# Kernel optimization log

Measured on AMD Instinct MI355X. Metric: run time of the kernel, lower is better.

The kernel has to match this reference:

```python
import jax, jax.numpy as jnp
import numpy as np

B, P, ENC, DEC, EMB, ATT, FFN, V, MAXLEN = 64, 196, 512, 512, 256, 128, 1024, 2000, 160
T = MAXLEN - 1
EPS = 1e-5

def _k(i):
    return jax.random.fold_in(jax.random.key(0), i)

def _w(i, shape):
    return jax.random.normal(_k(i), shape, jnp.float32) * 0.02

def setup_inputs() -> dict:
    lens = jnp.concatenate([jnp.array([MAXLEN]), jax.random.randint(_k(2), (B - 1,), 2, MAXLEN + 1)])
    return {
        "encoder_out": jax.random.normal(_k(0), (B, P, ENC), jnp.float32),
        "encoded_captions": jax.random.randint(_k(1), (B, MAXLEN), 0, V),
        "caption_lengths": lens,
        "enc_att_w": _w(3, (ATT, ENC)), "enc_att_b": _w(4, (ATT,)),
        "dec_att_w": _w(5, (ATT, DEC)), "dec_att_b": _w(6, (ATT,)),
        "full_att_w": _w(7, (1, ATT)), "full_att_b": _w(8, (1,)),
        "gate_w1": _w(9, (ATT, DEC)), "gate_b1": _w(10, (ATT,)),
        "gate_w2": _w(11, (1, ATT)), "gate_b2": _w(12, (1,)),
        "emb": jax.random.uniform(_k(13), (V, EMB), jnp.float32, -0.1, 0.1),
        "gru1_wih": _w(14, (3 * DEC, EMB + ENC)), "gru1_whh": _w(15, (3 * DEC, DEC)),
        "gru1_bih": _w(16, (3 * DEC,)), "gru1_bhh": _w(17, (3 * DEC,)),
        "gru2_wih": _w(18, (3 * DEC, DEC)), "gru2_whh": _w(19, (3 * DEC, DEC)),
        "gru2_bih": _w(20, (3 * DEC,)), "gru2_bhh": _w(21, (3 * DEC,)),
        "proj_w": _w(22, (DEC, EMB + ENC)), "proj_b": _w(23, (DEC,)),
        "ln1_g": jnp.ones((DEC,), jnp.float32), "ln1_b": jnp.zeros((DEC,), jnp.float32),
        "ln2_g": jnp.ones((DEC,), jnp.float32), "ln2_b": jnp.zeros((DEC,), jnp.float32),
        "ffn_w1": _w(24, (FFN, DEC)), "ffn_b1": jnp.zeros((FFN,), jnp.float32),
        "ffn_w2": _w(25, (V, FFN)), "ffn_b2": jnp.zeros((V,), jnp.float32),
    }

def _gru(x, h, wih, whh, bih, bhh):
    gi = x @ wih.T + bih
    gh = h @ whh.T + bhh
    ir, iz, ig = jnp.split(gi, 3, axis=-1)
    hr, hz, hg = jnp.split(gh, 3, axis=-1)
    r = jax.nn.sigmoid(ir + hr)
    z = jax.nn.sigmoid(iz + hz)
    n = jnp.tanh(ig + r * hg)
    return (1.0 - z) * n + z * h

def _ln(x, g, b):
    m = x.mean(-1, keepdims=True)
    v = x.var(-1, keepdims=True)
    return (x - m) / jnp.sqrt(v + EPS) * g + b

def _decode(encoder_out, encoded_captions, caption_lengths,
            enc_att_w, enc_att_b, dec_att_w, dec_att_b, full_att_w, full_att_b,
            gate_w1, gate_b1, gate_w2, gate_b2, emb,
            gru1_wih, gru1_whh, gru1_bih, gru1_bhh,
            gru2_wih, gru2_whh, gru2_bih, gru2_bhh,
            proj_w, proj_b, ln1_g, ln1_b, ln2_g, ln2_b,
            ffn_w1, ffn_b1, ffn_w2, ffn_b2):
    # sort by caption length descending (packed-sequence style)
    order = jnp.argsort(-caption_lengths)
    enc = encoder_out[order]                       # [B,P,ENC]
    caps = encoded_captions[order]                 # [B,MAXLEN]
    dec_lens = caption_lengths[order] - 1          # [B]
    att1 = enc @ enc_att_w.T + enc_att_b           # [B,P,ATT] (loop-invariant)
    xs = jnp.swapaxes(emb[caps[:, :T]], 0, 1)      # [T,B,EMB] teacher forcing (p=1.0)
    masks = (jnp.arange(T)[:, None] < dec_lens[None, :]).astype(enc.dtype)  # [T,B]

    def step(carry, inp):
        h1, h2 = carry
        x_t, m = inp                               # [B,EMB], [B]
        att2 = h2 @ dec_att_w.T + dec_att_b        # [B,ATT]
        e = (jax.nn.relu(att1 + att2[:, None, :]) @ full_att_w.T + full_att_b)[..., 0]  # [B,P]
        alpha = jax.nn.softmax(e, axis=1)
        awe = jnp.einsum('bpe,bp->be', enc, alpha)
        gate = jax.nn.sigmoid(jax.nn.relu(h2 @ gate_w1.T + gate_b1) @ gate_w2.T + gate_b2)  # [B,1]
        awe = awe * gate
        gin = jnp.concatenate([x_t, awe], axis=1)  # [B,EMB+ENC]
        h1_new = _gru(gin, h1, gru1_wih, gru1_whh, gru1_bih, gru1_bhh)
        h1_res = _ln(h1_new + gin @ proj_w.T + proj_b, ln1_g, ln1_b)
        h2_new = _gru(h1_res, h2, gru2_wih, gru2_whh, gru2_bih, gru2_bhh)
        h2_res = _ln(h2_new + h1_res, ln2_g, ln2_b)  # dropout is identity (eval)
        preds = jax.nn.relu(h2_res @ ffn_w1.T + ffn_b1) @ ffn_w2.T + ffn_b2  # [B,V]
        mc = m[:, None]
        h1 = jnp.where(mc > 0, h1_new, h1)
        h2 = jnp.where(mc > 0, h2_new, h2)
        return (h1, h2), (preds * mc, alpha * mc)

    h0 = jnp.zeros((enc.shape[0], DEC), enc.dtype)
    _, (preds, alphas) = jax.lax.scan(step, (h0, h0), (xs, masks))
    predictions = jnp.swapaxes(preds, 0, 1)        # [B,T,V]
    alphas = jnp.swapaxes(alphas, 0, 1)            # [B,T,P]
    return predictions, caps, dec_lens, alphas, order

def reference(encoder_out, encoded_captions, caption_lengths,
              enc_att_w, enc_att_b, dec_att_w, dec_att_b, full_att_w, full_att_b,
              gate_w1, gate_b1, gate_w2, gate_b2, emb,
              gru1_wih, gru1_whh, gru1_bih, gru1_bhh,
              gru2_wih, gru2_whh, gru2_bih, gru2_bhh,
              proj_w, proj_b, ln1_g, ln1_b, ln2_g, ln2_b,
              ffn_w1, ffn_b1, ffn_w2, ffn_b2):
    return _decode(encoder_out, encoded_captions, caption_lengths,
                   enc_att_w, enc_att_b, dec_att_w, dec_att_b, full_att_w, full_att_b,
                   gate_w1, gate_b1, gate_w2, gate_b2, emb,
                   gru1_wih, gru1_whh, gru1_bih, gru1_bhh,
                   gru2_wih, gru2_whh, gru2_bih, gru2_bhh,
                   proj_w, proj_b, ln1_g, ln1_b, ln2_g, ln2_b,
                   ffn_w1, ffn_b1, ffn_w2, ffn_b2)
```

## Files before the change

### kernel.cpp

```cpp
#include <hip/hip_runtime.h>
#include <math.h>

#define B 64
#define P 196
#define ENCD 512
#define DECD 512
#define EMBD 256
#define ATTD 128
#define FFND 1024
#define VV 2000
#define MAXLEN 160
#define TSTEPS 159
#define EPS 1e-5f

#define OUT_PRED ((size_t)0)
#define OUT_CAPS ((size_t)(B * TSTEPS * VV))
#define OUT_DECL (OUT_CAPS + (size_t)(B * MAXLEN))
#define OUT_ALPH (OUT_DECL + (size_t)B)
#define OUT_ORDR (OUT_ALPH + (size_t)(B * TSTEPS * P))


struct Ctx {
  const float* enc; const int* caps_in; const int* lens_in;
  const float* eaw; const float* eab; const float* daw; const float* dab;
  const float* faw; const float* fab;
  const float* gw1; const float* gb1; const float* gw2; const float* gb2;
  const float* emb;
  const float* wih1; const float* whh1; const float* bih1; const float* bhh1;
  const float* wih2; const float* whh2; const float* bih2; const float* bhh2;
  const float* projw; const float* projb;
  const float* ln1g; const float* ln1b; const float* ln2g; const float* ln2b;
  const float* fw1; const float* fb1; const float* fw2; const float* fb2;
  int* leafs; int* root;
  int* order_i; int* declen; int* caps_s;
  float* EaT; float* att1;
  float* h1; float* h2; float* v1; float* v2;
  float* gin; float* fgr; float* gh1g; float* gh2g; float* att2acc;
  float* stats1; float* stats2;
  float* WA; float* WB; float* WC; float* WD; float* Watt;
  float* Sf; float* cbf; float* Sg; float* cbg;
  float* out;
};

__device__ __forceinline__ float sigf(float x) { return 1.f / (1.f + __expf(-x)); }

__device__ __forceinline__ float ld4(const float* p) {
  unsigned int u = __hip_atomic_load((const unsigned int*)p, __ATOMIC_RELAXED, __HIP_MEMORY_SCOPE_AGENT);
  return __uint_as_float(u);
}
__device__ __forceinline__ void st4(float* p, float v) {
  __hip_atomic_store((unsigned int*)p, __float_as_uint(v), __ATOMIC_RELAXED, __HIP_MEMORY_SCOPE_AGENT);
}
__device__ __forceinline__ void st8(float* p, float a, float b2) {
  unsigned long long v = ((unsigned long long)__float_as_uint(b2) << 32) | (unsigned long long)__float_as_uint(a);
  __hip_atomic_store((unsigned long long*)p, v, __ATOMIC_RELAXED, __HIP_MEMORY_SCOPE_AGENT);
}
__device__ __forceinline__ void atomF(float* p, float v) {
  __hip_atomic_fetch_add(p, v, __ATOMIC_RELAXED, __HIP_MEMORY_SCOPE_AGENT);
}
__device__ __forceinline__ float4 ldg16(const float* p) {
  float4 d;
  asm volatile("global_load_dwordx4 %0, %1, off sc0 sc1" : "=v"(d) : "v"(p));
  return d;
}
__device__ __forceinline__ void vmwait() { asm volatile("s_waitcnt vmcnt(0)" ::: "memory"); }

__device__ __forceinline__ float pfl(const float* p) {
  float v;
  asm volatile("global_load_dword %0, %1, off" : "=v"(v) : "v"(p));
  return v;
}
__device__ __forceinline__ void pfsink8(float a, float b, float c2, float d,
                                        float e, float f, float g2, float h) {
  asm volatile("" :: "v"(a), "v"(b), "v"(c2), "v"(d), "v"(e), "v"(f), "v"(g2), "v"(h));
}
__device__ __forceinline__ void pfsink2(float a, float b) {
  asm volatile("" :: "v"(a), "v"(b));
}

__device__ __forceinline__ unsigned short tobf(float x) {
  unsigned int u = __float_as_uint(x);
  u += 0x7fffu + ((u >> 16) & 1u);
  return (unsigned short)(u >> 16);
}
__device__ __forceinline__ float frombf(unsigned short s) {
  return __uint_as_float(((unsigned int)s) << 16);
}


__global__ void k_order(Ctx c) {
  __shared__ int lens[B];
  int tid = threadIdx.x;
  lens[tid] = c.lens_in[tid];
  __syncthreads();
  int li = lens[tid];
  int pos = 0;
  for (int j = 0; j < B; ++j) {
    int lj = lens[j];
    pos += (lj > li || (lj == li && j < tid)) ? 1 : 0;
  }
  c.order_i[pos] = tid;
  c.declen[pos] = li - 1;
  c.out[OUT_ORDR + pos] = (float)tid;
  c.out[OUT_DECL + pos] = (float)(li - 1);
}

__global__ __launch_bounds__(256) void k_caps(Ctx c) {
  int idx = blockIdx.x * 256 + threadIdx.x;
  if (idx < B * MAXLEN) {
    int b = idx / MAXLEN, t = idx - b * MAXLEN;
    int v = c.caps_in[c.order_i[b] * MAXLEN + t];
    c.caps_s[idx] = v;
    c.out[OUT_CAPS + idx] = (float)v;
  }
}

__global__ __launch_bounds__(256) void k_eat(Ctx c) {
  int idx = blockIdx.x * 256 + threadIdx.x;
  if (idx < 128 * 512) {
    int k = idx >> 7, d = idx & 127;
    c.EaT[(size_t)k * 128 + d] = c.eaw[(size_t)d * 512 + k];
  }
}

__global__ __launch_bounds__(256) void k_att1(Ctx c) {
  __shared__ float Xs[8 * 512];
  int tid = threadIdx.x;
  int r0 = blockIdx.x * 8;
  for (int idx = tid; idx < 8 * 512; idx += 256) {
    int rr = idx >> 9, k = idx & 511;
    int r = r0 + rr;
    int b = r / P, p = r - b * P;
    int ob = c.order_i[b];
    Xs[idx] = c.enc[((size_t)(ob * P + p)) * ENCD + k];
  }
  __syncthreads();
  int d = tid >> 1, kh = tid & 1;
  float acc[8];
#pragma unroll
  for (int rr = 0; rr < 8; ++rr) acc[rr] = 0.f;
  int kbase = kh * 256;
  for (int k = 0; k < 256; ++k) {
    float w = c.EaT[(size_t)(kbase + k) * 128 + d];
#pragma unroll
    for (int rr = 0; rr < 8; ++rr) acc[rr] = fmaf(w, Xs[rr * 512 + kbase + k], acc[rr]);
  }
#pragma unroll
  for (int rr = 0; rr < 8; ++rr) {
    acc[rr] += __shfl_xor(acc[rr], 1);
    if (kh == 0) c.att1[(size_t)(r0 + rr) * 128 + d] = acc[rr];
  }
}

__global__ __launch_bounds__(256) void k_wpa(Ctx c) {
  int s = blockIdx.x;
  float* dst = c.WA + (size_t)s * 65536;
  for (int idx = threadIdx.x; idx < 65536; idx += 256) {
    int kb = idx >> 9, r = idx & 511, cc = r >> 2, jj = r & 3;
    int col = s * 128 + cc, k = kb * 4 + jj;
    float v;
    if (col < 1536) v = c.whh1[(size_t)col * 512 + k];
    else if (col < 3072) v = c.whh2[(size_t)(col - 1536) * 512 + k];
    else v = c.ln2g[k] * c.fw1[(size_t)(col - 3072) * 512 + k];
    dst[idx] = v;
  }
}

__global__ __launch_bounds__(256) void k_wpb(Ctx c) {
  int s = blockIdx.x;
  float* dst = c.WB + (size_t)s * 49152;
  for (int idx = threadIdx.x; idx < 49152; idx += 256) {
    int kb = idx >> 8, r = idx & 255, cc = r >> 2, jj = r & 3;
    int u = s * 64 + cc, k = kb * 4 + jj;
    int d = u >> 2, comp = u & 3;
    dst[idx] = (comp < 3) ? c.wih1[(size_t)(comp * 512 + d) * 768 + k]
                          : c.projw[(size_t)d * 768 + k];
  }
}

__global__ __launch_bounds__(256) void k_wpc(Ctx c) {
  int s = blockIdx.x;
  float* dst = c.WC + (size_t)s * 24576;
  for (int idx = threadIdx.x; idx < 24576; idx += 256) {
    int kb = idx / 192, r = idx - kb * 192, cc = r >> 2, jj = r & 3;
    int u = s * 48 + cc, k = kb * 4 + jj;
    int d = u / 3, comp = u - d * 3;
    dst[idx] = c.ln1g[k] * c.wih2[(size_t)(comp * 512 + d) * 512 + k];
  }
}

__global__ __launch_bounds__(256) void k_wpd(Ctx c) {
  int s = blockIdx.x;
  float* dst = c.WD + (size_t)s * 65536;
  for (int idx = threadIdx.x; idx < 65536; idx += 256) {
    int kb = idx >> 8, r = idx & 255, cc = r >> 2, jj = r & 3;
    int vcol = s * 64 + cc, k = kb * 4 + jj;
    dst[idx] = (vcol < 2000) ? c.fw2[(size_t)vcol * 1024 + k] : 0.f;
  }
}

__global__ __launch_bounds__(256) void k_watt(Ctx c) {
  int ks = blockIdx.x;
  float* dst = c.Watt + (size_t)ks * 16384;
  for (int idx = threadIdx.x; idx < 16384; idx += 256) {
    int kb = idx >> 10, r = idx & 1023, cc = r >> 2, jj = r & 3;
    int k = ks * 64 + kb * 4 + jj;
    dst[idx] = (cc < 128) ? c.daw[(size_t)cc * 512 + k] : c.gw1[(size_t)(cc - 128) * 512 + k];
  }
}

__global__ __launch_bounds__(256) void k_consts(Ctx c) {
  __shared__ float r1[256], r2[256];
  int i = blockIdx.x, tid = threadIdx.x;
  float a = 0.f, b2 = 0.f;
  if (i < 1024) {
    const float* w = c.fw1 + (size_t)i * 512;
    for (int k = tid; k < 512; k += 256) { a = fmaf(c.ln2g[k], w[k], a); b2 = fmaf(c.ln2b[k], w[k], b2); }
  } else {
    const float* w = c.wih2 + (size_t)(i - 1024) * 512;
    for (int k = tid; k < 512; k += 256) { a = fmaf(c.ln1g[k], w[k], a); b2 = fmaf(c.ln1b[k], w[k], b2); }
  }
  r1[tid] = a; r2[tid] = b2;
  __syncthreads();
  for (int s = 128; s > 0; s >>= 1) {
    if (tid < s) { r1[tid] += r1[tid + s]; r2[tid] += r2[tid + s]; }
    __syncthreads();
  }
  if (tid == 0) {
    if (i < 1024) { c.Sf[i] = r1[0]; c.cbf[i] = r2[0] + c.fb1[i]; }
    else { c.Sg[i - 1024] = r1[0]; c.cbg[i - 1024] = r2[0] + c.bih2[i - 1024]; }
  }
}


__device__ __forceinline__ void gridbar(int* leafs, int* root, int ph) {
  __builtin_amdgcn_s_waitcnt(0);
  __syncthreads();
  if (threadIdx.x == 0) {
    int old = __hip_atomic_fetch_add(&leafs[(blockIdx.x & 7) * 32], 1,
                                     __ATOMIC_RELAXED, __HIP_MEMORY_SCOPE_AGENT);
    if (old == ph * 32 - 1)
      __hip_atomic_fetch_add(root, 1, __ATOMIC_RELAXED, __HIP_MEMORY_SCOPE_AGENT);
    while (__hip_atomic_load(root, __ATOMIC_RELAXED, __HIP_MEMORY_SCOPE_AGENT) < ph * 8)
      __builtin_amdgcn_s_sleep(1);
  }
  __syncthreads();
}

__global__ __launch_bounds__(512) void persist(Ctx c) {
  __shared__ unsigned short att1L[196 * 130];
  __shared__ unsigned short encL[196 * 128];
  __shared__ float SH[12288];
  __shared__ float eL[256];
  __shared__ float alphaL[256];
  __shared__ float att2sL[128], fawL[128], dabL[128], gb1L[128], gw2L[128];
  __shared__ float wred[16];
  __shared__ float sstat[16];
  __shared__ int declenI[64];
  __shared__ float gb2v, fabv;

  const int g = blockIdx.x;
  const int tid = threadIdx.x;
  const int cg = g & 31;
  const int rg = g >> 5;
  const int r0 = rg * 8;
  const int bA = g >> 2, q = g & 3;
  const int kc = tid >> 6;
  const int ct = tid & 63;

  if (tid < 128) {
    fawL[tid] = c.faw[tid];
    dabL[tid] = c.dab[tid] + c.eab[tid];
    gb1L[tid] = c.gb1[tid];
    gw2L[tid] = c.gw2[tid];
  }
  if (tid == 0) { gb2v = c.gb2[0]; fabv = c.fab[0]; }
  if (tid < 64) declenI[tid] = c.declen[tid];
  {
    const int ob = c.order_i[bA];
    for (int idx = tid; idx < 196 * 128; idx += 512) {
      int p = idx >> 7, j = idx & 127;
      att1L[p * 130 + j] = tobf(c.att1[((size_t)bA * P + p) * 128 + j]);
      encL[idx] = tobf(c.enc[((size_t)(ob * P + p)) * 512 + q * 128 + j]);
    }
  }
  __syncthreads();

  int ph = 0;
  for (int t = 0; t < MAXLEN; ++t) {
    {
      float* XS = SH;
      float* RED = SH + 4096;
      const float* hsrc = ((cg < 12) ? c.h1 : (cg < 24) ? c.h2 : c.v2) + (size_t)r0 * 512;
      float4 s0 = ldg16(hsrc + tid * 4);
      float4 s1 = ldg16(hsrc + 2048 + tid * 4);
      if (tid < 8) {
        int slot = (t + 1) & 1;
        float a = ld4(c.stats2 + slot * 128 + (r0 + tid) * 2);
        float b2 = ld4(c.stats2 + slot * 128 + (r0 + tid) * 2 + 1);
        float m = a * (1.f / 512.f);
        float va = b2 * (1.f / 512.f) - m * m;
        sstat[tid] = m; sstat[8 + tid] = rsqrtf(va + EPS);
      }
      vmwait();
      *(float4*)(XS + tid * 4) = s0;
      *(float4*)(XS + 2048 + tid * 4) = s1;
      __syncthreads();

      {
        const float* wp = c.WA + (size_t)cg * 65536 + kc * 8192 + ct * 4;
        const float* xb = XS + kc * 64;
        float acc[8][2];
#pragma unroll
        for (int r = 0; r < 8; ++r) { acc[r][0] = 0.f; acc[r][1] = 0.f; }
#pragma unroll 4
        for (int i = 0; i < 16; ++i) {
          float4 w0 = *(const float4*)(wp + i * 512);
          float4 w1 = *(const float4*)(wp + i * 512 + 256);
#pragma unroll
          for (int r = 0; r < 8; ++r) {
            float4 x = *(const float4*)(xb + r * 512 + i * 4);
            acc[r][0] = fmaf(w0.x, x.x, fmaf(w0.y, x.y, fmaf(w0.z, x.z, fmaf(w0.w, x.w, acc[r][0]))));
            acc[r][1] = fmaf(w1.x, x.x, fmaf(w1.y, x.y, fmaf(w1.z, x.z, fmaf(w1.w, x.w, acc[r][1]))));
          }
        }
#pragma unroll
        for (int r = 0; r < 8; ++r) {
          RED[(kc * 8 + r) * 128 + ct] = acc[r][0];
          RED[(kc * 8 + r) * 128 + ct + 64] = acc[r][1];
        }
      }
      if (cg >= 16 && cg < 24) {
        const int ks_att = cg - 16;
        const int ct2 = tid >> 1, half = tid & 1;
        const float* wp = c.Watt + (size_t)ks_att * 16384 + half * 8192 + ct2 * 4;
        const float* xb = XS + ks_att * 64 + half * 32;
        float a[8];
#pragma unroll
        for (int r = 0; r < 8; ++r) a[r] = 0.f;
#pragma unroll
        for (int i = 0; i < 8; ++i) {
          float4 w = *(const float4*)(wp + i * 1024);
#pragma unroll
          for (int r = 0; r < 8; ++r) {
            float4 x = *(const float4*)(xb + r * 512 + i * 4);
            a[r] = fmaf(w.x, x.x, fmaf(w.y, x.y, fmaf(w.z, x.z, fmaf(w.w, x.w, a[r]))));
          }
        }
#pragma unroll
        for (int r = 0; r < 8; ++r) {
          a[r] += __shfl_xor(a[r], 1);
          if (half == 0) atomF(c.att2acc + (r0 + r) * 256 + ct2, a[r]);
        }
      }
      float pw[8];
      {
        const float* pb = c.WD + (size_t)cg * 65536 + tid * 16;
#pragma unroll
        for (int i = 0; i < 8; ++i) pw[i] = pfl(pb + i * 8192);
      }
      __syncthreads();
      {
        int row = tid >> 6, cp = (tid & 63) * 2;
        float s0_ = 0.f, s1_ = 0.f;
#pragma unroll
        for (int k8 = 0; k8 < 8; ++k8) {
          float2 v = *(const float2*)(RED + (k8 * 8 + row) * 128 + cp);
          s0_ += v.x; s1_ += v.y;
        }
        int bb = r0 + row;
        int gcol = cg * 128 + cp;
        if (cg < 12) st8(c.gh1g + bb * 1536 + gcol, s0_, s1_);
        else if (cg < 24) st8(c.gh2g + bb * 1536 + (gcol - 1536), s0_, s1_);
        else {
          int cf = gcol - 3072;
          float m2 = sstat[row], i2 = sstat[8 + row];
          float v0 = i2 * (s0_ - m2 * c.Sf[cf]) + c.cbf[cf];
          float v1v = i2 * (s1_ - m2 * c.Sf[cf + 1]) + c.cbf[cf + 1];
          st8(c.fgr + bb * 1024 + cf, fmaxf(v0, 0.f), fmaxf(v1v, 0.f));
        }
      }
      pfsink8(pw[0], pw[1], pw[2], pw[3], pw[4], pw[5], pw[6], pw[7]);
    }
    gridbar(c.leafs, c.root, ++ph);

    {
      float* XS = SH;
      float* RED = SH + 8192;
      const float* fsrc = c.fgr + (size_t)r0 * 1024;
      float4 s0 = ldg16(fsrc + tid * 4);
      float4 s1 = ldg16(fsrc + 2048 + tid * 4);
      float4 s2 = ldg16(fsrc + 4096 + tid * 4);
      float4 s3 = ldg16(fsrc + 6144 + tid * 4);
      float a2r = 0.f, g1r = 0.f;
      if (tid < 128) {
        a2r = ld4(c.att2acc + bA * 256 + tid);
        g1r = ld4(c.att2acc + bA * 256 + 128 + tid);
      }
      if (g == 0) {
        int sl = t & 1;
        if (tid < 128) st4(c.stats1 + sl * 128 + tid, 0.f);
        else if (tid < 256) st4(c.stats2 + sl * 128 + (tid - 128), 0.f);
      }
      vmwait();
      *(float4*)(XS + tid * 4) = s0;
      *(float4*)(XS + 2048 + tid * 4) = s1;
      *(float4*)(XS + 4096 + tid * 4) = s2;
      *(float4*)(XS + 6144 + tid * 4) = s3;
      if (tid < 128) {
        att2sL[tid] = a2r + dabL[tid];
        float g1 = fmaxf(g1r + gb1L[tid], 0.f);
        float gv = g1 * gw2L[tid];
#pragma unroll
        for (int w = 1; w < 64; w <<= 1) gv += __shfl_xor(gv, w);
        if ((tid & 63) == 0) wred[tid >> 6] = gv;
      }
      __syncthreads();

      {
        const float* wp = c.WD + (size_t)cg * 65536 + kc * 8192 + ct * 4;
        const float* xb = XS + kc * 128;
        float acc[8];
#pragma unroll
        for (int r = 0; r < 8; ++r) acc[r] = 0.f;
#pragma unroll 4
        for (int i = 0; i < 32; ++i) {
          float4 w = *(const float4*)(wp + i * 256);
#pragma unroll
          for (int r = 0; r < 8; ++r) {
            float4 x = *(const float4*)(xb + r * 1024 + i * 4);
            acc[r] = fmaf(w.x, x.x, fmaf(w.y, x.y, fmaf(w.z, x.z, fmaf(w.w, x.w, acc[r]))));
          }
        }
#pragma unroll
        for (int r = 0; r < 8; ++r) RED[(kc * 8 + r) * 64 + ct] = acc[r];
      }
      float pw[6];
      {
        const float* pb = c.WB + (size_t)cg * 49152 + tid * 16;
#pragma unroll
        for (int i = 0; i < 6; ++i) pw[i] = pfl(pb + i * 8192);
      }
      __syncthreads();
      {
        int row = tid >> 6, cl = tid & 63;
        float s = 0.f;
#pragma unroll
        for (int k8 = 0; k8 < 8; ++k8) s += RED[(k8 * 8 + row) * 64 + cl];
        int bb = r0 + row, vcol = cg * 64 + cl;
        if (vcol < 2000 && t > 0 && (t - 1) < declenI[bb])
          c.out[OUT_PRED + ((size_t)bb * TSTEPS + (t - 1)) * VV + vcol] = s + c.fb2[vcol];
      }
      {
        int p = tid >> 1, jh = tid & 1;
        float e = 0.f;
        if (p < 196) {
          const unsigned short* ap = att1L + p * 130 + jh * 64;
#pragma unroll 8
          for (int j = 0; j < 64; ++j)
            e = fmaf(fmaxf(frombf(ap[j]) + att2sL[jh * 64 + j], 0.f), fawL[jh * 64 + j], e);
        }
        e += __shfl_xor(e, 1);
        if (jh == 0 && p < 196) eL[p] = e + fabv;
      }
      __syncthreads();
      float ev = (tid < 196) ? eL[tid] : -3.0e38f;
      if (tid < 256) {
        float mv = ev;
#pragma unroll
        for (int w = 1; w < 64; w <<= 1) mv = fmaxf(mv, __shfl_xor(mv, w));
        if ((tid & 63) == 0) wred[2 + (tid >> 6)] = mv;
      }
      __syncthreads();
      float mx = fmaxf(fmaxf(wred[2], wred[3]), fmaxf(wred[4], wred[5]));
      float ex = (tid < 196) ? __expf(ev - mx) : 0.f;
      if (tid < 256) {
        float sv = ex;
#pragma unroll
        for (int w = 1; w < 64; w <<= 1) sv += __shfl_xor(sv, w);
        if ((tid & 63) == 0) wred[6 + (tid >> 6)] = sv;
      }
      __syncthreads();
      float inv = 1.f / (wred[6] + wred[7] + wred[8] + wred[9]);
      float gate = sigf(wred[0] + wred[1] + gb2v);
      if (tid < 256) alphaL[tid] = ex * inv;
      if (q == 0 && tid < 196 && t < declenI[bA])
        c.out[OUT_ALPH + ((size_t)bA * TSTEPS + t) * P + tid] = ex * inv;
      __syncthreads();
      {
        int el = tid & 127, pq = tid >> 7;
        const unsigned short* ep2 = encL + (size_t)(pq * 49) * 128 + el;
        const float* alp = alphaL + pq * 49;
        float s_ = 0.f;
#pragma unroll
        for (int i = 0; i < 49; ++i) s_ = fmaf(alp[i], frombf(ep2[(size_t)i * 128]), s_);
        RED[tid] = s_;
      }
      __syncthreads();
      if (tid < 128) {
        float aw = RED[tid] + RED[128 + tid] + RED[256 + tid] + RED[384 + tid];
        st4(c.gin + bA * 768 + 256 + q * 128 + tid, aw * gate);
      }
      if (q == 1 && tid < 256) {
        int tok = c.caps_s[bA * MAXLEN + t];
        st4(c.gin + bA * 768 + tid, c.emb[(size_t)tok * 256 + tid]);
      }
      pfsink8(pw[0], pw[1], pw[2], pw[3], pw[4], pw[5], pw[0], pw[1]);
    }
    gridbar(c.leafs, c.root, ++ph);

    {
      float* XS = SH;
      float* RED = SH + 6144;
      const float* gsrc = c.gin + (size_t)r0 * 768;
      float4 s0 = ldg16(gsrc + tid * 4);
      float4 s1 = ldg16(gsrc + 2048 + tid * 4);
      float4 s2 = ldg16(gsrc + 4096 + tid * 4);
      if (g < 32) st4(c.att2acc + g * 512 + tid, 0.f);
      vmwait();
      *(float4*)(XS + tid * 4) = s0;
      *(float4*)(XS + 2048 + tid * 4) = s1;
      *(float4*)(XS + 4096 + tid * 4) = s2;
      __syncthreads();

      {
        const float* wp = c.WB + (size_t)cg * 49152 + kc * 6144 + ct * 4;
        const float* xb = XS + kc * 96;
        float acc[8];
#pragma unroll
        for (int r = 0; r < 8; ++r) acc[r] = 0.f;
#pragma unroll 4
        for (int i = 0; i < 24; ++i) {
          float4 w = *(const float4*)(wp + i * 256);
#pragma unroll
          for (int r = 0; r < 8; ++r) {
            float4 x = *(const float4*)(xb + r * 768 + i * 4);
            acc[r] = fmaf(w.x, x.x, fmaf(w.y, x.y, fmaf(w.z, x.z, fmaf(w.w, x.w, acc[r]))));
          }
        }
#pragma unroll
        for (int r = 0; r < 8; ++r) RED[(kc * 8 + r) * 64 + ct] = acc[r];
      }
      float pw[3];
      {
        const float* pb = c.WC + (size_t)cg * 24576 + tid * 16;
#pragma unroll
        for (int i = 0; i < 3; ++i) pw[i] = pfl(pb + i * 8192);
      }
      __syncthreads();
      if (tid < 128) {
        int row = tid >> 4, dl = tid & 15;
        int bb = r0 + row, d = cg * 16 + dl;
        float gi0 = 0.f, gi1 = 0.f, gi2v = 0.f, gi3 = 0.f;
#pragma unroll
        for (int k8 = 0; k8 < 8; ++k8) {
          float4 v = *(const float4*)(RED + (k8 * 8 + row) * 64 + dl * 4);
          gi0 += v.x; gi1 += v.y; gi2v += v.z; gi3 += v.w;
        }
        float gir = gi0 + c.bih1[d];
        float giz = gi1 + c.bih1[512 + d];
        float gig = gi2v + c.bih1[1024 + d];
        float pj = gi3 + c.projb[d];
        float hr = ld4(c.gh1g + bb * 1536 + d) + c.bhh1[d];
        float hz = ld4(c.gh1g + bb * 1536 + 512 + d) + c.bhh1[512 + d];
        float hg = ld4(c.gh1g + bb * 1536 + 1024 + d) + c.bhh1[1024 + d];
        float r_ = sigf(gir + hr);
        float z_ = sigf(giz + hz);
        float n_ = tanhf(gig + r_ * hg);
        float hold = ld4(c.h1 + bb * 512 + d);
        float hnew = (1.f - z_) * n_ + z_ * hold;
        st4(c.h1 + bb * 512 + d, (t < declenI[bb]) ? hnew : hold);
        float v1v = hnew + pj;
        st4(c.v1 + bb * 512 + d, v1v);
        float ss = v1v, sq = v1v * v1v;
#pragma unroll
        for (int w = 1; w < 16; w <<= 1) { ss += __shfl_xor(ss, w); sq += __shfl_xor(sq, w); }
        if (dl == 0) {
          atomF(c.stats1 + (t & 1) * 128 + bb * 2, ss);
          atomF(c.stats1 + (t & 1) * 128 + bb * 2 + 1, sq);
        }
      }
      pfsink8(pw[0], pw[1], pw[2], pw[0], pw[1], pw[2], pw[0], pw[1]);
    }
    gridbar(c.leafs, c.root, ++ph);

    {
      float* XS = SH;
      float* RED = SH + 4096;
      const float* vsrc = c.v1 + (size_t)r0 * 512;
      float4 s0 = ldg16(vsrc + tid * 4);
      float4 s1 = ldg16(vsrc + 2048 + tid * 4);
      if (tid < 8) {
        float a = ld4(c.stats1 + (t & 1) * 128 + (r0 + tid) * 2);
        float b2 = ld4(c.stats1 + (t & 1) * 128 + (r0 + tid) * 2 + 1);
        float m = a * (1.f / 512.f);
        float va = b2 * (1.f / 512.f) - m * m;
        sstat[tid] = m; sstat[8 + tid] = rsqrtf(va + EPS);
      }
      vmwait();
      *(float4*)(XS + tid * 4) = s0;
      *(float4*)(XS + 2048 + tid * 4) = s1;
      __syncthreads();

      if (ct < 48) {
        const float* wp = c.WC + (size_t)cg * 24576 + kc * 3072 + ct * 4;
        const float* xb = XS + kc * 64;
        float acc[8];
#pragma unroll
        for (int r = 0; r < 8; ++r) acc[r] = 0.f;
#pragma unroll 4
        for (int i = 0; i < 16; ++i) {
          float4 w = *(const float4*)(wp + i * 192);
#pragma unroll
          for (int r = 0; r < 8; ++r) {
            float4 x = *(const float4*)(xb + r * 512 + i * 4);
            acc[r] = fmaf(w.x, x.x, fmaf(w.y, x.y, fmaf(w.z, x.z, fmaf(w.w, x.w, acc[r]))));
          }
        }
#pragma unroll
        for (int r = 0; r < 8; ++r) RED[(kc * 8 + r) * 48 + ct] = acc[r];
      }
      float pw[8];
      {
        const float* pb = c.WA + (size_t)cg * 65536 + tid * 16;
#pragma unroll
        for (int i = 0; i < 8; ++i) pw[i] = pfl(pb + i * 8192);
      }
      float pa0 = 0.f, pa1 = 0.f;
      if (cg >= 16 && cg < 24) {
        const float* pb = c.Watt + (size_t)(cg - 16) * 16384 + tid * 16;
        pa0 = pfl(pb);
        pa1 = pfl(pb + 8192);
      }
      __syncthreads();
      if (tid < 128) {
        int row = tid >> 4, dl = tid & 15;
        int bb = r0 + row, d = cg * 16 + dl;
        float gi0 = 0.f, gi1 = 0.f, gi2v = 0.f;
#pragma unroll
        for (int k8 = 0; k8 < 8; ++k8) {
          const float* rp = RED + (k8 * 8 + row) * 48 + dl * 3;
          gi0 += rp[0]; gi1 += rp[1]; gi2v += rp[2];
        }
        float m1 = sstat[row], i1 = sstat[8 + row];
        float gir = i1 * (gi0 - m1 * c.Sg[d]) + c.cbg[d];
        float giz = i1 * (gi1 - m1 * c.Sg[512 + d]) + c.cbg[512 + d];
        float gig = i1 * (gi2v - m1 * c.Sg[1024 + d]) + c.cbg[1024 + d];
        float hr = ld4(c.gh2g + bb * 1536 + d) + c.bhh2[d];
        float hz = ld4(c.gh2g + bb * 1536 + 512 + d) + c.bhh2[512 + d];
        float hg = ld4(c.gh2g + bb * 1536 + 1024 + d) + c.bhh2[1024 + d];
        float r_ = sigf(gir + hr);
        float z_ = sigf(giz + hz);
        float n_ = tanhf(gig + r_ * hg);
        float hold = ld4(c.h2 + bb * 512 + d);
        float hnew = (1.f - z_) * n_ + z_ * hold;
        st4(c.h2 + bb * 512 + d, (t < declenI[bb]) ? hnew : hold);
        float h1r = (XS[row * 512 + d] - m1) * i1 * c.ln1g[d] + c.ln1b[d];
        float v2v = hnew + h1r;
        st4(c.v2 + bb * 512 + d, v2v);
        float ss = v2v, sq = v2v * v2v;
#pragma unroll
        for (int w = 1; w < 16; w <<= 1) { ss += __shfl_xor(ss, w); sq += __shfl_xor(sq, w); }
        if (dl == 0) {
          atomF(c.stats2 + (t & 1) * 128 + bb * 2, ss);
          atomF(c.stats2 + (t & 1) * 128 + bb * 2 + 1, sq);
        }
      }
      pfsink8(pw[0], pw[1], pw[2], pw[3], pw[4], pw[5], pw[6], pw[7]);
      pfsink2(pa0, pa1);
    }
    gridbar(c.leafs, c.root, ++ph);
  }
}

extern "C" void kernel_launch(void* const* d_in, const int* in_sizes, int n_in,
                              void* d_out, int out_size, void* d_ws, size_t ws_size,
                              hipStream_t stream) {
  (void)in_sizes; (void)n_in; (void)ws_size;
  Ctx c;
  c.enc = (const float*)d_in[0];
  c.caps_in = (const int*)d_in[1];
  c.lens_in = (const int*)d_in[2];
  c.eaw = (const float*)d_in[3];
  c.eab = (const float*)d_in[4];
  c.daw = (const float*)d_in[5];
  c.dab = (const float*)d_in[6];
  c.faw = (const float*)d_in[7];
  c.fab = (const float*)d_in[8];
  c.gw1 = (const float*)d_in[9];
  c.gb1 = (const float*)d_in[10];
  c.gw2 = (const float*)d_in[11];
  c.gb2 = (const float*)d_in[12];
  c.emb = (const float*)d_in[13];
  c.wih1 = (const float*)d_in[14];
  c.whh1 = (const float*)d_in[15];
  c.bih1 = (const float*)d_in[16];
  c.bhh1 = (const float*)d_in[17];
  c.wih2 = (const float*)d_in[18];
  c.whh2 = (const float*)d_in[19];
  c.bih2 = (const float*)d_in[20];
  c.bhh2 = (const float*)d_in[21];
  c.projw = (const float*)d_in[22];
  c.projb = (const float*)d_in[23];
  c.ln1g = (const float*)d_in[24];
  c.ln1b = (const float*)d_in[25];
  c.ln2g = (const float*)d_in[26];
  c.ln2b = (const float*)d_in[27];
  c.fw1 = (const float*)d_in[28];
  c.fb1 = (const float*)d_in[29];
  c.fw2 = (const float*)d_in[30];
  c.fb2 = (const float*)d_in[31];
  c.out = (float*)d_out;

  char* wp_ = (char*)d_ws;
  auto alloc = [&](size_t bytes) -> char* {
    char* p = wp_;
    wp_ += (bytes + 255) & ~(size_t)255;
    return p;
  };
  char* zbase = wp_;
  c.leafs = (int*)alloc(256 * 4);
  c.root = (int*)alloc(256);
  c.h1 = (float*)alloc((size_t)B * 512 * 4);
  c.h2 = (float*)alloc((size_t)B * 512 * 4);
  c.stats1 = (float*)alloc(2 * 64 * 2 * 4);
  c.stats2 = (float*)alloc(2 * 64 * 2 * 4);
  c.att2acc = (float*)alloc((size_t)B * 256 * 4);
  c.v2 = (float*)alloc((size_t)B * 512 * 4);
  size_t zbytes = (size_t)(wp_ - zbase);

  c.order_i = (int*)alloc(B * 4);
  c.declen = (int*)alloc(B * 4);
  c.caps_s = (int*)alloc((size_t)B * MAXLEN * 4);
  c.EaT = (float*)alloc((size_t)512 * 128 * 4);
  c.att1 = (float*)alloc((size_t)B * P * 128 * 4);
  c.v1 = (float*)alloc((size_t)B * 512 * 4);
  c.gin = (float*)alloc((size_t)B * 768 * 4);
  c.fgr = (float*)alloc((size_t)B * 1024 * 4);
  c.gh1g = (float*)alloc((size_t)B * 1536 * 4);
  c.gh2g = (float*)alloc((size_t)B * 1536 * 4);
  c.WA = (float*)alloc((size_t)32 * 65536 * 4);
  c.WB = (float*)alloc((size_t)32 * 49152 * 4);
  c.WC = (float*)alloc((size_t)32 * 24576 * 4);
  c.WD = (float*)alloc((size_t)32 * 65536 * 4);
  c.Watt = (float*)alloc((size_t)8 * 16384 * 4);
  c.Sf = (float*)alloc(1024 * 4);
  c.cbf = (float*)alloc(1024 * 4);
  c.Sg = (float*)alloc(1536 * 4);
  c.cbg = (float*)alloc(1536 * 4);

  hipMemsetAsync(d_out, 0, (size_t)out_size * 4, stream);
  hipMemsetAsync(zbase, 0, zbytes, stream);

  k_order<<<1, 64, 0, stream>>>(c);
  k_caps<<<(B * MAXLEN + 255) / 256, 256, 0, stream>>>(c);
  k_eat<<<(128 * 512 + 255) / 256, 256, 0, stream>>>(c);
  k_att1<<<(B * P) / 8, 256, 0, stream>>>(c);
  k_wpa<<<32, 256, 0, stream>>>(c);
  k_wpb<<<32, 256, 0, stream>>>(c);
  k_wpc<<<32, 256, 0, stream>>>(c);
  k_wpd<<<32, 256, 0, stream>>>(c);
  k_watt<<<8, 256, 0, stream>>>(c);
  k_consts<<<2560, 256, 0, stream>>>(c);

  persist<<<256, 512, 0, stream>>>(c);
}
```

Baseline: 14.38 ms.

## Store packed recurrent weights as bf16 and drop cross-phase L2 prefetches

Converts the four repacked weight matrices (WA, WB, WC, WD) from fp32 to packed bf16 pairs. They are unpacked to fp32 in registers inside the per-step matvec loops, which halves the weight bytes streamed in every phase of the persistent recurrent kernel. The LayerNorm-folded constant Sg/Sf is computed from bf16-rounded products so it stays consistent with the rounded weights. The prefetch loads that warmed the next phase's weights into cache are removed. This trades weight precision for bandwidth and risks larger numerical error accumulating over 159 recurrent steps.

```diff
diff --git a/kernel.cpp b/kernel.cpp
--- a/kernel.cpp
+++ b/kernel.cpp
@@ -37,7 +37,8 @@
   float* h1; float* h2; float* v1; float* v2;
   float* gin; float* fgr; float* gh1g; float* gh2g; float* att2acc;
   float* stats1; float* stats2;
-  float* WA; float* WB; float* WC; float* WD; float* Watt;
+  unsigned int* WA; unsigned int* WB; unsigned int* WC; unsigned int* WD;
+  float* Watt;
   float* Sf; float* cbf; float* Sg; float* cbg;
   float* out;
 };
@@ -65,19 +66,6 @@
 }
 __device__ __forceinline__ void vmwait() { asm volatile("s_waitcnt vmcnt(0)" ::: "memory"); }
 
-__device__ __forceinline__ float pfl(const float* p) {
-  float v;
-  asm volatile("global_load_dword %0, %1, off" : "=v"(v) : "v"(p));
-  return v;
-}
-__device__ __forceinline__ void pfsink8(float a, float b, float c2, float d,
-                                        float e, float f, float g2, float h) {
-  asm volatile("" :: "v"(a), "v"(b), "v"(c2), "v"(d), "v"(e), "v"(f), "v"(g2), "v"(h));
-}
-__device__ __forceinline__ void pfsink2(float a, float b) {
-  asm volatile("" :: "v"(a), "v"(b));
-}
-
 __device__ __forceinline__ unsigned short tobf(float x) {
   unsigned int u = __float_as_uint(x);
   u += 0x7fffu + ((u >> 16) & 1u);
@@ -85,6 +73,13 @@
 }
 __device__ __forceinline__ float frombf(unsigned short s) {
   return __uint_as_float(((unsigned int)s) << 16);
+}
+__device__ __forceinline__ unsigned int pack2bf(float a, float b) {
+  return (unsigned int)tobf(a) | ((unsigned int)tobf(b) << 16);
+}
+__device__ __forceinline__ void bf2(unsigned int u, float& a, float& b) {
+  a = __uint_as_float(u << 16);
+  b = __uint_as_float(u & 0xffff0000u);
 }
 
 
@@ -152,50 +147,64 @@
   }
 }
 
+__device__ __forceinline__ float wa_elem(const Ctx& c, int col, int k) {
+  if (col < 1536) return c.whh1[(size_t)col * 512 + k];
+  if (col < 3072) return c.whh2[(size_t)(col - 1536) * 512 + k];
+  return c.ln2g[k] * c.fw1[(size_t)(col - 3072) * 512 + k];
+}
+
 __global__ __launch_bounds__(256) void k_wpa(Ctx c) {
   int s = blockIdx.x;
-  float* dst = c.WA + (size_t)s * 65536;
-  for (int idx = threadIdx.x; idx < 65536; idx += 256) {
-    int kb = idx >> 9, r = idx & 511, cc = r >> 2, jj = r & 3;
-    int col = s * 128 + cc, k = kb * 4 + jj;
-    float v;
-    if (col < 1536) v = c.whh1[(size_t)col * 512 + k];
-    else if (col < 3072) v = c.whh2[(size_t)(col - 1536) * 512 + k];
-    else v = c.ln2g[k] * c.fw1[(size_t)(col - 3072) * 512 + k];
-    dst[idx] = v;
-  }
+  unsigned int* dst = c.WA + (size_t)s * 32768;
+  for (int idx = threadIdx.x; idx < 32768; idx += 256) {
+    int kb8 = idx >> 9, r = idx & 511, cc = r >> 2, jw = r & 3;
+    int col = s * 128 + cc, k0 = kb8 * 8 + jw * 2;
+    dst[idx] = pack2bf(wa_elem(c, col, k0), wa_elem(c, col, k0 + 1));
+  }
+}
+
+__device__ __forceinline__ float wb_elem(const Ctx& c, int u, int k) {
+  int d = u >> 2, comp = u & 3;
+  return (comp < 3) ? c.wih1[(size_t)(comp * 512 + d) * 768 + k]
+                    : c.projw[(size_t)d * 768 + k];
 }
 
 __global__ __launch_bounds__(256) void k_wpb(Ctx c) {
   int s = blockIdx.x;
-  float* dst = c.WB + (size_t)s * 49152;
-  for (int idx = threadIdx.x; idx < 49152; idx += 256) {
-    int kb = idx >> 8, r = idx & 255, cc = r >> 2, jj = r & 3;
-    int u = s * 64 + cc, k = kb * 4 + jj;
-    int d = u >> 2, comp = u & 3;
-    dst[idx] = (comp < 3) ? c.wih1[(size_t)(comp * 512 + d) * 768 + k]
-                          : c.projw[(size_t)d * 768 + k];
-  }
+  unsigned int* dst = c.WB + (size_t)s * 24576;
+  for (int idx = threadIdx.x; idx < 24576; idx += 256) {
+    int kb8 = idx >> 8, r = idx & 255, cc = r >> 2, jw = r & 3;
+    int u = s * 64 + cc, k0 = kb8 * 8 + jw * 2;
+    dst[idx] = pack2bf(wb_elem(c, u, k0), wb_elem(c, u, k0 + 1));
+  }
+}
+
+__device__ __forceinline__ float wc_elem(const Ctx& c, int u, int k) {
+  int d = u / 3, comp = u - d * 3;
+  return c.ln1g[k] * c.wih2[(size_t)(comp * 512 + d) * 512 + k];
 }
 
 __global__ __launch_bounds__(256) void k_wpc(Ctx c) {
   int s = blockIdx.x;
-  float* dst = c.WC + (size_t)s * 24576;
-  for (int idx = threadIdx.x; idx < 24576; idx += 256) {
-    int kb = idx / 192, r = idx - kb * 192, cc = r >> 2, jj = r & 3;
-    int u = s * 48 + cc, k = kb * 4 + jj;
-    int d = u / 3, comp = u - d * 3;
-    dst[idx] = c.ln1g[k] * c.wih2[(size_t)(comp * 512 + d) * 512 + k];
-  }
+  unsigned int* dst = c.WC + (size_t)s * 12288;
+  for (int idx = threadIdx.x; idx < 12288; idx += 256) {
+    int kb8 = idx / 192, r = idx - kb8 * 192, cc = r >> 2, jw = r & 3;
+    int u = s * 48 + cc, k0 = kb8 * 8 + jw * 2;
+    dst[idx] = pack2bf(wc_elem(c, u, k0), wc_elem(c, u, k0 + 1));
+  }
+}
+
+__device__ __forceinline__ float wd_elem(const Ctx& c, int vcol, int k) {
+  return (vcol < 2000) ? c.fw2[(size_t)vcol * 1024 + k] : 0.f;
 }
 
 __global__ __launch_bounds__(256) void k_wpd(Ctx c) {
   int s = blockIdx.x;
-  float* dst = c.WD + (size_t)s * 65536;
-  for (int idx = threadIdx.x; idx < 65536; idx += 256) {
-    int kb = idx >> 8, r = idx & 255, cc = r >> 2, jj = r & 3;
-    int vcol = s * 64 + cc, k = kb * 4 + jj;
-    dst[idx] = (vcol < 2000) ? c.fw2[(size_t)vcol * 1024 + k] : 0.f;
+  unsigned int* dst = c.WD + (size_t)s * 32768;
+  for (int idx = threadIdx.x; idx < 32768; idx += 256) {
+    int kb8 = idx >> 8, r = idx & 255, cc = r >> 2, jw = r & 3;
+    int vcol = s * 64 + cc, k0 = kb8 * 8 + jw * 2;
+    dst[idx] = pack2bf(wd_elem(c, vcol, k0), wd_elem(c, vcol, k0 + 1));
   }
 }
 
@@ -215,10 +224,16 @@
   float a = 0.f, b2 = 0.f;
   if (i < 1024) {
     const float* w = c.fw1 + (size_t)i * 512;
-    for (int k = tid; k < 512; k += 256) { a = fmaf(c.ln2g[k], w[k], a); b2 = fmaf(c.ln2b[k], w[k], b2); }
+    for (int k = tid; k < 512; k += 256) {
+      a += frombf(tobf(c.ln2g[k] * w[k]));
+      b2 = fmaf(c.ln2b[k], w[k], b2);
+    }
   } else {
     const float* w = c.wih2 + (size_t)(i - 1024) * 512;
-    for (int k = tid; k < 512; k += 256) { a = fmaf(c.ln1g[k], w[k], a); b2 = fmaf(c.ln1b[k], w[k], b2); }
+    for (int k = tid; k < 512; k += 256) {
+      a += frombf(tobf(c.ln1g[k] * w[k]));
+      b2 = fmaf(c.ln1b[k], w[k], b2);
+    }
   }
   r1[tid] = a; r2[tid] = b2;
   __syncthreads();
@@ -308,20 +323,28 @@
       __syncthreads();
 
       {
-        const float* wp = c.WA + (size_t)cg * 65536 + kc * 8192 + ct * 4;
+        const unsigned int* wp = c.WA + (size_t)cg * 32768 + (size_t)kc * 4096 + ct * 4;
         const float* xb = XS + kc * 64;
         float acc[8][2];
 #pragma unroll
         for (int r = 0; r < 8; ++r) { acc[r][0] = 0.f; acc[r][1] = 0.f; }
-#pragma unroll 4
-        for (int i = 0; i < 16; ++i) {
-          float4 w0 = *(const float4*)(wp + i * 512);
-          float4 w1 = *(const float4*)(wp + i * 512 + 256);
+#pragma unroll 2
+        for (int i = 0; i < 8; ++i) {
+          uint4 u0 = *(const uint4*)(wp + i * 512);
+          uint4 u1 = *(const uint4*)(wp + i * 512 + 256);
+          float wa[8], wb[8];
+          bf2(u0.x, wa[0], wa[1]); bf2(u0.y, wa[2], wa[3]);
+          bf2(u0.z, wa[4], wa[5]); bf2(u0.w, wa[6], wa[7]);
+          bf2(u1.x, wb[0], wb[1]); bf2(u1.y, wb[2], wb[3]);
+          bf2(u1.z, wb[4], wb[5]); bf2(u1.w, wb[6], wb[7]);
 #pragma unroll
           for (int r = 0; r < 8; ++r) {
-            float4 x = *(const float4*)(xb + r * 512 + i * 4);
-            acc[r][0] = fmaf(w0.x, x.x, fmaf(w0.y, x.y, fmaf(w0.z, x.z, fmaf(w0.w, x.w, acc[r][0]))));
-            acc[r][1] = fmaf(w1.x, x.x, fmaf(w1.y, x.y, fmaf(w1.z, x.z, fmaf(w1.w, x.w, acc[r][1]))));
+            float4 x0 = *(const float4*)(xb + r * 512 + i * 8);
+            float4 x1 = *(const float4*)(xb + r * 512 + i * 8 + 4);
+            acc[r][0] = fmaf(wa[0], x0.x, fmaf(wa[1], x0.y, fmaf(wa[2], x0.z, fmaf(wa[3], x0.w, acc[r][0]))));
+            acc[r][0] = fmaf(wa[4], x1.x, fmaf(wa[5], x1.y, fmaf(wa[6], x1.z, fmaf(wa[7], x1.w, acc[r][0]))));
+            acc[r][1] = fmaf(wb[0], x0.x, fmaf(wb[1], x0.y, fmaf(wb[2], x0.z, fmaf(wb[3], x0.w, acc[r][1]))));
+            acc[r][1] = fmaf(wb[4], x1.x, fmaf(wb[5], x1.y, fmaf(wb[6], x1.z, fmaf(wb[7], x1.w, acc[r][1]))));
           }
         }
 #pragma unroll
@@ -352,12 +375,6 @@
           a[r] += __shfl_xor(a[r], 1);
           if (half == 0) atomF(c.att2acc + (r0 + r) * 256 + ct2, a[r]);
         }
-      }
-      float pw[8];
-      {
-        const float* pb = c.WD + (size_t)cg * 65536 + tid * 16;
-#pragma unroll
-        for (int i = 0; i < 8; ++i) pw[i] = pfl(pb + i * 8192);
       }
       __syncthreads();
       {
@@ -380,7 +397,6 @@
           st8(c.fgr + bb * 1024 + cf, fmaxf(v0, 0.f), fmaxf(v1v, 0.f));
         }
       }
-      pfsink8(pw[0], pw[1], pw[2], pw[3], pw[4], pw[5], pw[6], pw[7]);
     }
     gridbar(c.leafs, c.root, ++ph);
 
@@ -418,28 +434,27 @@
       __syncthreads();
 
       {
-        const float* wp = c.WD + (size_t)cg * 65536 + kc * 8192 + ct * 4;
+        const unsigned int* wp = c.WD + (size_t)cg * 32768 + (size_t)kc * 4096 + ct * 4;
         const float* xb = XS + kc * 128;
         float acc[8];
 #pragma unroll
         for (int r = 0; r < 8; ++r) acc[r] = 0.f;
 #pragma unroll 4
-        for (int i = 0; i < 32; ++i) {
-          float4 w = *(const float4*)(wp + i * 256);
+        for (int i = 0; i < 16; ++i) {
+          uint4 u = *(const uint4*)(wp + i * 256);
+          float w8[8];
+          bf2(u.x, w8[0], w8[1]); bf2(u.y, w8[2], w8[3]);
+          bf2(u.z, w8[4], w8[5]); bf2(u.w, w8[6], w8[7]);
 #pragma unroll
           for (int r = 0; r < 8; ++r) {
-            float4 x = *(const float4*)(xb + r * 1024 + i * 4);
-            acc[r] = fmaf(w.x, x.x, fmaf(w.y, x.y, fmaf(w.z, x.z, fmaf(w.w, x.w, acc[r]))));
+            float4 x0 = *(const float4*)(xb + r * 1024 + i * 8);
+            float4 x1 = *(const float4*)(xb + r * 1024 + i * 8 + 4);
+            acc[r] = fmaf(w8[0], x0.x, fmaf(w8[1], x0.y, fmaf(w8[2], x0.z, fmaf(w8[3], x0.w, acc[r]))));
+            acc[r] = fmaf(w8[4], x1.x, fmaf(w8[5], x1.y, fmaf(w8[6], x1.z, fmaf(w8[7], x1.w, acc[r]))));
           }
         }
 #pragma unroll
         for (int r = 0; r < 8; ++r) RED[(kc * 8 + r) * 64 + ct] = acc[r];
-      }
-      float pw[6];
-      {
-        const float* pb = c.WB + (size_t)cg * 49152 + tid * 16;
-#pragma unroll
-        for (int i = 0; i < 6; ++i) pw[i] = pfl(pb + i * 8192);
       }
       __syncthreads();
       {
@@ -505,7 +520,6 @@
         int tok = c.caps_s[bA * MAXLEN + t];
         st4(c.gin + bA * 768 + tid, c.emb[(size_t)tok * 256 + tid]);
       }
-      pfsink8(pw[0], pw[1], pw[2], pw[3], pw[4], pw[5], pw[0], pw[1]);
     }
     gridbar(c.leafs, c.root, ++ph);
 
@@ -524,28 +538,27 @@
       __syncthreads();
 
       {
-        const float* wp = c.WB + (size_t)cg * 49152 + kc * 6144 + ct * 4;
+        const unsigned int* wp = c.WB + (size_t)cg * 24576 + (size_t)kc * 3072 + ct * 4;
         const float* xb = XS + kc * 96;
         float acc[8];
 #pragma unroll
         for (int r = 0; r < 8; ++r) acc[r] = 0.f;
 #pragma unroll 4
-        for (int i = 0; i < 24; ++i) {
-          float4 w = *(const float4*)(wp + i * 256);
+        for (int i = 0; i < 12; ++i) {
+          uint4 u = *(const uint4*)(wp + i * 256);
+          float w8[8];
+          bf2(u.x, w8[0], w8[1]); bf2(u.y, w8[2], w8[3]);
+          bf2(u.z, w8[4], w8[5]); bf2(u.w, w8[6], w8[7]);
 #pragma unroll
           for (int r = 0; r < 8; ++r) {
-            float4 x = *(const float4*)(xb + r * 768 + i * 4);
-            acc[r] = fmaf(w.x, x.x, fmaf(w.y, x.y, fmaf(w.z, x.z, fmaf(w.w, x.w, acc[r]))));
+            float4 x0 = *(const float4*)(xb + r * 768 + i * 8);
+            float4 x1 = *(const float4*)(xb + r * 768 + i * 8 + 4);
+            acc[r] = fmaf(w8[0], x0.x, fmaf(w8[1], x0.y, fmaf(w8[2], x0.z, fmaf(w8[3], x0.w, acc[r]))));
+            acc[r] = fmaf(w8[4], x1.x, fmaf(w8[5], x1.y, fmaf(w8[6], x1.z, fmaf(w8[7], x1.w, acc[r]))));
           }
         }
 #pragma unroll
         for (int r = 0; r < 8; ++r) RED[(kc * 8 + r) * 64 + ct] = acc[r];
-      }
-      float pw[3];
-      {
-        const float* pb = c.WC + (size_t)cg * 24576 + tid * 16;
-#pragma unroll
-        for (int i = 0; i < 3; ++i) pw[i] = pfl(pb + i * 8192);
       }
       __syncthreads();
       if (tid < 128) {
@@ -580,7 +593,6 @@
           atomF(c.stats1 + (t & 1) * 128 + bb * 2 + 1, sq);
         }
       }
-      pfsink8(pw[0], pw[1], pw[2], pw[0], pw[1], pw[2], pw[0], pw[1]);
     }
     gridbar(c.leafs, c.root, ++ph);
 
@@ -603,34 +615,27 @@
       __syncthreads();
 
       if (ct < 48) {
-        const float* wp = c.WC + (size_t)cg * 24576 + kc * 3072 + ct * 4;
+        const unsigned int* wp = c.WC + (size_t)cg * 12288 + (size_t)kc * 1536 + ct * 4;
         const float* xb = XS + kc * 64;
         float acc[8];
 #pragma unroll
         for (int r = 0; r < 8; ++r) acc[r] = 0.f;
-#pragma unroll 4
-        for (int i = 0; i < 16; ++i) {
-          float4 w = *(const float4*)(wp + i * 192);
+#pragma unroll 2
+        for (int i = 0; i < 8; ++i) {
+          uint4 u = *(const uint4*)(wp + i * 192);
+          float w8[8];
+          bf2(u.x, w8[0], w8[1]); bf2(u.y, w8[2], w8[3]);
+          bf2(u.z, w8[4], w8[5]); bf2(u.w, w8[6], w8[7]);
 #pragma unroll
           for (int r = 0; r < 8; ++r) {
-            float4 x = *(const float4*)(xb + r * 512 + i * 4);
-            acc[r] = fmaf(w.x, x.x, fmaf(w.y, x.y, fmaf(w.z, x.z, fmaf(w.w, x.w, acc[r]))));
+            float4 x0 = *(const float4*)(xb + r * 512 + i * 8);
+            float4 x1 = *(const float4*)(xb + r * 512 + i * 8 + 4);
+            acc[r] = fmaf(w8[0], x0.x, fmaf(w8[1], x0.y, fmaf(w8[2], x0.z, fmaf(w8[3], x0.w, acc[r]))));
+            acc[r] = fmaf(w8[4], x1.x, fmaf(w8[5], x1.y, fmaf(w8[6], x1.z, fmaf(w8[7], x1.w, acc[r]))));
           }
         }
 #pragma unroll
         for (int r = 0; r < 8; ++r) RED[(kc * 8 + r) * 48 + ct] = acc[r];
-      }
-      float pw[8];
-      {
-        const float* pb = c.WA + (size_t)cg * 65536 + tid * 16;
-#pragma unroll
-        for (int i = 0; i < 8; ++i) pw[i] = pfl(pb + i * 8192);
-      }
-      float pa0 = 0.f, pa1 = 0.f;
-      if (cg >= 16 && cg < 24) {
-        const float* pb = c.Watt + (size_t)(cg - 16) * 16384 + tid * 16;
-        pa0 = pfl(pb);
-        pa1 = pfl(pb + 8192);
       }
       __syncthreads();
       if (tid < 128) {
@@ -666,8 +671,6 @@
           atomF(c.stats2 + (t & 1) * 128 + bb * 2 + 1, sq);
         }
       }
-      pfsink8(pw[0], pw[1], pw[2], pw[3], pw[4], pw[5], pw[6], pw[7]);
-      pfsink2(pa0, pa1);
     }
     gridbar(c.leafs, c.root, ++ph);
   }
@@ -739,10 +742,10 @@
   c.fgr = (float*)alloc((size_t)B * 1024 * 4);
   c.gh1g = (float*)alloc((size_t)B * 1536 * 4);
   c.gh2g = (float*)alloc((size_t)B * 1536 * 4);
-  c.WA = (float*)alloc((size_t)32 * 65536 * 4);
-  c.WB = (float*)alloc((size_t)32 * 49152 * 4);
-  c.WC = (float*)alloc((size_t)32 * 24576 * 4);
-  c.WD = (float*)alloc((size_t)32 * 65536 * 4);
+  c.WA = (unsigned int*)alloc((size_t)32 * 32768 * 4);
+  c.WB = (unsigned int*)alloc((size_t)32 * 24576 * 4);
+  c.WC = (unsigned int*)alloc((size_t)32 * 12288 * 4);
+  c.WD = (unsigned int*)alloc((size_t)32 * 32768 * 4);
   c.Watt = (float*)alloc((size_t)8 * 16384 * 4);
   c.Sf = (float*)alloc(1024 * 4);
   c.cbf = (float*)alloc(1024 * 4);
```

Measured after the change: 11.72 ms. 18.5% less time.
